# Kernel optimization log

Measured on AMD Instinct MI355X. Metric: run time of the kernel, lower is better.

The kernel has to match this reference:

```python
import jax, jax.numpy as jnp
import numpy as np

N = 12288      # num_nodes
D = 128        # seg_emb
NUM_GRAPHS = 48
NUM_CLS = 27   # classes 24,25,26 are excluded by the module


def setup_inputs() -> dict:
    key = jax.random.key(0)
    k1, k2, k3, k4 = jax.random.split(key, 4)
    z1 = jax.random.normal(k1, (N, D), dtype=jnp.float32)
    z2 = jax.random.normal(k2, (N, D), dtype=jnp.float32)
    cls_label = jax.random.randint(k3, (N,), 0, NUM_CLS, dtype=jnp.int32)
    batch = jnp.sort(jax.random.randint(k4, (N,), 0, NUM_GRAPHS, dtype=jnp.int32))
    return {"z1": z1, "z2": z2, "cls_label": cls_label, "batch": batch}


def reference(z1, z2, cls_label, batch):
    # Pairwise validity mask: same graph AND same class AND class not in {24,25,26}.
    # This reproduces the nested gather->matmul->scatter loops: each (graph, class)
    # block of z1 @ z2.T is kept, everything else stays zero. Single-node classes
    # (skipped in the original) only contribute a diagonal entry, which is zeroed.
    same_graph = batch[:, None] == batch[None, :]            # [N, N]
    same_cls = cls_label[:, None] == cls_label[None, :]      # [N, N]
    excluded = (cls_label >= 24) & (cls_label <= 26)         # [N]
    mask = same_graph & same_cls & ~excluded[:, None]

    scores = jnp.matmul(z1, z2.T)                            # [N, N] inner products
    out = jnp.where(mask, scores, jnp.float32(0.0))
    n = out.shape[0]
    idx = jnp.arange(n)
    out = out.at[idx, idx].set(0.0)                          # zero the diagonal
    return out
```

## Files before the change

### kernel.cpp

```cpp
#include <hip/hip_runtime.h>

#define NN 12288
#define DD 128

typedef float v4f __attribute__((ext_vector_type(4)));

__global__ __launch_bounds__(256) void segdec_fused(
    const float* __restrict__ z1, const float* __restrict__ z2,
    const int* __restrict__ cls, const int* __restrict__ batch,
    float* __restrict__ out)
{
    const int i   = blockIdx.x;
    const int tid = threadIdx.x;
    v4f* __restrict__ orow = reinterpret_cast<v4f*>(out + (size_t)i * NN);
    const v4f zero4 = {0.f, 0.f, 0.f, 0.f};

    const int cls_i = cls[i];
    if (cls_i >= 24) {
        #pragma unroll
        for (int k = 0; k < 12; ++k)
            __builtin_nontemporal_store(zero4, &orow[tid + (k << 8)]);
        return;
    }

    const int batch_i = batch[i];
    int lo, hi;
    {
        int l = 0, r = NN;
        while (l < r) { int m = (l + r) >> 1; if (batch[m] <  batch_i) l = m + 1; else r = m; }
        lo = l;
        r = NN;
        while (l < r) { int m = (l + r) >> 1; if (batch[m] <= batch_i) l = m + 1; else r = m; }
        hi = l;
    }

    unsigned band_mask = 0u;
    #pragma unroll
    for (int k = 0; k < 12; ++k) {
        const int f4 = tid + (k << 8);
        const int c0 = f4 << 2;
        if (c0 < hi && c0 + 4 > lo) {
            band_mask |= (1u << k);
        } else {
            __builtin_nontemporal_store(zero4, &orow[f4]);
        }
    }

    if (band_mask) {
        const v4f* __restrict__ za = reinterpret_cast<const v4f*>(z1 + (size_t)i * DD);
        while (band_mask) {
            const int k = __builtin_ctz(band_mask);
            band_mask &= band_mask - 1;
            const int f4 = tid + (k << 8);
            const int c0 = f4 << 2;
            float vv[4] = {0.f, 0.f, 0.f, 0.f};
            #pragma unroll
            for (int u = 0; u < 4; ++u) {
                const int j = c0 + u;
                if (j >= lo && j < hi && j != i && cls[j] == cls_i) {
                    const v4f* __restrict__ zb =
                        reinterpret_cast<const v4f*>(z2 + (size_t)j * DD);
                    float s = 0.f;
                    #pragma unroll
                    for (int d = 0; d < DD / 4; ++d) {
                        const v4f a = za[d];
                        const v4f b = zb[d];
                        s = fmaf(a.x, b.x, s);
                        s = fmaf(a.y, b.y, s);
                        s = fmaf(a.z, b.z, s);
                        s = fmaf(a.w, b.w, s);
                    }
                    vv[u] = s;
                }
            }
            const v4f v = {vv[0], vv[1], vv[2], vv[3]};
            __builtin_nontemporal_store(v, &orow[f4]);
        }
    }
}

extern "C" void kernel_launch(void* const* d_in, const int* in_sizes, int n_in,
                              void* d_out, int out_size, void* d_ws, size_t ws_size,
                              hipStream_t stream) {
    const float* z1    = (const float*)d_in[0];
    const float* z2    = (const float*)d_in[1];
    const int*   cls   = (const int*)d_in[2];
    const int*   batch = (const int*)d_in[3];
    float*       out   = (float*)d_out;

    segdec_fused<<<NN, 256, 0, stream>>>(z1, z2, cls, batch, out);
}
```

Before: 645.5 us.

## Split output zeroing into a dedicated streaming kernel and band-only fill kernel

Replaces the single per-row fused kernel with two launches. A grid-strided kernel zeros the entire output, then a band kernel with 128 threads per row computes only the same-graph column range and overwrites it. This aims to turn most of the work into a uniform bulk memset-style write and to remove the per-row band-mask logic and load imbalance. In exchange, the band region is written twice, the nontemporal store hints are dropped, and a second launch is added.

Result: slower. 673.7 us (+4.4%).

```diff
diff --git a/kernel.cpp b/kernel.cpp
--- a/kernel.cpp
+++ b/kernel.cpp
@@ -3,79 +3,67 @@
 #define NN 12288
 #define DD 128
 
+#define ZGRID 4096
+#define ZITER 36
+
 typedef float v4f __attribute__((ext_vector_type(4)));
 
-__global__ __launch_bounds__(256) void segdec_fused(
+__global__ __launch_bounds__(256) void zero_out(float* __restrict__ out)
+{
+    v4f* __restrict__ o4 = reinterpret_cast<v4f*>(out);
+    const v4f z = {0.f, 0.f, 0.f, 0.f};
+    const size_t base = (size_t)blockIdx.x * 256 + threadIdx.x;
+    #pragma unroll
+    for (int k = 0; k < ZITER; ++k)
+        o4[base + (size_t)k * ((size_t)ZGRID * 256)] = z;
+}
+
+__global__ __launch_bounds__(128) void band_fill(
     const float* __restrict__ z1, const float* __restrict__ z2,
     const int* __restrict__ cls, const int* __restrict__ batch,
     float* __restrict__ out)
 {
-    const int i   = blockIdx.x;
-    const int tid = threadIdx.x;
-    v4f* __restrict__ orow = reinterpret_cast<v4f*>(out + (size_t)i * NN);
-    const v4f zero4 = {0.f, 0.f, 0.f, 0.f};
-
+    const int i = blockIdx.x;
     const int cls_i = cls[i];
-    if (cls_i >= 24) {
-        #pragma unroll
-        for (int k = 0; k < 12; ++k)
-            __builtin_nontemporal_store(zero4, &orow[tid + (k << 8)]);
-        return;
-    }
+    if (cls_i >= 24) return;
 
     const int batch_i = batch[i];
-    int lo, hi;
-    {
-        int l = 0, r = NN;
-        while (l < r) { int m = (l + r) >> 1; if (batch[m] <  batch_i) l = m + 1; else r = m; }
-        lo = l;
-        r = NN;
-        while (l < r) { int m = (l + r) >> 1; if (batch[m] <= batch_i) l = m + 1; else r = m; }
-        hi = l;
-    }
+    int l = 0, r = NN;
+    while (l < r) { const int m = (l + r) >> 1; if (batch[m] <  batch_i) l = m + 1; else r = m; }
+    const int lo = l;
+    r = NN;
+    while (l < r) { const int m = (l + r) >> 1; if (batch[m] <= batch_i) l = m + 1; else r = m; }
+    const int hi = l;
 
-    unsigned band_mask = 0u;
-    #pragma unroll
-    for (int k = 0; k < 12; ++k) {
-        const int f4 = tid + (k << 8);
-        const int c0 = f4 << 2;
-        if (c0 < hi && c0 + 4 > lo) {
-            band_mask |= (1u << k);
-        } else {
-            __builtin_nontemporal_store(zero4, &orow[f4]);
+    const v4f* __restrict__ za  = reinterpret_cast<const v4f*>(z1 + (size_t)i * DD);
+    v4f* __restrict__ orow      = reinterpret_cast<v4f*>(out + (size_t)i * NN);
+
+    const int c0 = lo >> 2;
+    const int c1 = (hi - 1) >> 2;
+
+    for (int c = c0 + (int)threadIdx.x; c <= c1; c += 128) {
+        float vv[4] = {0.f, 0.f, 0.f, 0.f};
+        #pragma unroll
+        for (int u = 0; u < 4; ++u) {
+            const int j = (c << 2) | u;
+            if (j >= lo && j < hi && j != i && cls[j] == cls_i) {
+                const v4f* __restrict__ zb =
+                    reinterpret_cast<const v4f*>(z2 + (size_t)j * DD);
+                float s = 0.f;
+                #pragma unroll
+                for (int d = 0; d < DD / 4; ++d) {
+                    const v4f a = za[d];
+                    const v4f b = zb[d];
+                    s = fmaf(a.x, b.x, s);
+                    s = fmaf(a.y, b.y, s);
+                    s = fmaf(a.z, b.z, s);
+                    s = fmaf(a.w, b.w, s);
+                }
+                vv[u] = s;
+            }
         }
-    }
-
-    if (band_mask) {
-        const v4f* __restrict__ za = reinterpret_cast<const v4f*>(z1 + (size_t)i * DD);
-        while (band_mask) {
-            const int k = __builtin_ctz(band_mask);
-            band_mask &= band_mask - 1;
-            const int f4 = tid + (k << 8);
-            const int c0 = f4 << 2;
-            float vv[4] = {0.f, 0.f, 0.f, 0.f};
-            #pragma unroll
-            for (int u = 0; u < 4; ++u) {
-                const int j = c0 + u;
-                if (j >= lo && j < hi && j != i && cls[j] == cls_i) {
-                    const v4f* __restrict__ zb =
-                        reinterpret_cast<const v4f*>(z2 + (size_t)j * DD);
-                    float s = 0.f;
-                    #pragma unroll
-                    for (int d = 0; d < DD / 4; ++d) {
-                        const v4f a = za[d];
-                        const v4f b = zb[d];
-                        s = fmaf(a.x, b.x, s);
-                        s = fmaf(a.y, b.y, s);
-                        s = fmaf(a.z, b.z, s);
-                        s = fmaf(a.w, b.w, s);
-                    }
-                    vv[u] = s;
-                }
-            }
-            const v4f v = {vv[0], vv[1], vv[2], vv[3]};
-            __builtin_nontemporal_store(v, &orow[f4]);
-        }
+        const v4f v = {vv[0], vv[1], vv[2], vv[3]};
+        orow[c] = v;
     }
 }
 
@@ -88,5 +76,6 @@
     const int*   batch = (const int*)d_in[3];
     float*       out   = (float*)d_out;
 
-    segdec_fused<<<NN, 256, 0, stream>>>(z1, z2, cls, batch, out);
+    zero_out<<<ZGRID, 256, 0, stream>>>(out);
+    band_fill<<<NN, 128, 0, stream>>>(z1, z2, cls, batch, out);
 }
```
